# Performance work log

Hardware: AMD Instinct MI355X
Metric: run time of the kernel (lower is better)

The kernel has to match this reference:

```python
import jax, jax.numpy as jnp
import numpy as np

K_MAX, K_MIN = 12.0, 1.0
TEMP = 1.0
STE_ALPHA = 12.0
EPS = 1e-8

DIM, HID, KHID, WHID = 512, 2048, 128, 128
B, N = 8, 1024


def setup_inputs() -> dict:
    key = jax.random.key(0)
    ks = jax.random.split(key, 13)
    def lin(k, fan_in, shape):
        bound = 1.0 / np.sqrt(fan_in)
        return jax.random.uniform(k, shape, jnp.float32, -bound, bound)
    return {
        "x": jax.random.normal(ks[0], (B, N, DIM), jnp.float32),
        "fc1_w": lin(ks[1], DIM, (HID, DIM)),
        "fc1_b": lin(ks[2], DIM, (HID,)),
        "fc2_w": lin(ks[3], HID, (DIM, HID)),
        "fc2_b": lin(ks[4], HID, (DIM,)),
        "k1_w": lin(ks[5], DIM, (KHID, DIM)),
        "k1_b": lin(ks[6], DIM, (KHID,)),
        "k2_w": lin(ks[7], KHID, (3, KHID)),
        "k2_b": lin(ks[8], KHID, (3,)),
        "w1_w": lin(ks[9], DIM, (WHID, DIM)),
        "w1_b": lin(ks[10], DIM, (WHID,)),
        "w2_w": lin(ks[11], WHID, (3, WHID)),
        "w2_b": lin(ks[12], WHID, (3,)),
    }


def adaptive_knn_aggregate(h, k_cont):
    # h: (B,N,C), k_cont: (B,) continuous k in [k_min, k_max]
    sim = jnp.einsum("bnc,bmc->bnm", h, h) / TEMP          # (B,N,N)
    order = jnp.argsort(-sim, axis=-1)                      # descending
    rank = jnp.argsort(order, axis=-1).astype(h.dtype)      # rank 0 = most similar
    # soft top-k gate (STE-style sigmoid around k_cont)
    gate = jax.nn.sigmoid(STE_ALPHA * (k_cont[:, None, None] - (rank + 0.5)))
    attn = jax.nn.softmax(sim, axis=-1) * gate
    attn = attn / (attn.sum(axis=-1, keepdims=True) + EPS)
    return jnp.einsum("bnm,bmc->bnc", attn, h)


def reference(x, fc1_w, fc1_b, fc2_w, fc2_b, k1_w, k1_b, k2_w, k2_b,
              w1_w, w1_b, w2_w, w2_b):
    pooled = x.mean(axis=1)                                 # (B,C)
    # adaptive k values net
    kh = jax.nn.relu(pooled @ k1_w.T + k1_b)
    ratio = jax.nn.sigmoid(kh @ k2_w.T + k2_b)              # (B,3)
    k_cont = K_MIN + ratio * (K_MAX - K_MIN)
    # adaptive branch weights net
    wh = jax.nn.relu(pooled @ w1_w.T + w1_b)
    w = jax.nn.softmax(wh @ w2_w.T + w2_b, axis=-1)         # (B,3)
    # MLP (dropout p=0 -> identity)
    h = jax.nn.relu(x @ fc1_w.T + fc1_b)
    h = h @ fc2_w.T + fc2_b                                 # (B,N,C)
    # three KNN aggregation branches blended by w
    y = sum(adaptive_knn_aggregate(h, k_cont[:, i]) * w[:, i, None, None]
            for i in range(3))
    return y
```

## Files before the change

kernel.cpp:

```cpp
#include <hip/hip_runtime.h>
#include <math.h>

#define DIM_ 512
#define HID_ 2048
#define B_ 8
#define N_ 1024
#define ROWS_ 8192
#define TOPK 16

typedef __attribute__((ext_vector_type(8))) short short8;
typedef __attribute__((ext_vector_type(16))) float float16v;
typedef __attribute__((ext_vector_type(4))) float float4v;

__device__ __forceinline__ float sigm(float x) { return 1.f / (1.f + __expf(-x)); }

__device__ __forceinline__ short f2bf(float f) {
    unsigned u = __float_as_uint(f);
    u += 0x7FFF + ((u >> 16) & 1);
    return (short)(u >> 16);
}

__device__ __forceinline__ float bf2f(unsigned short s) {
    return __uint_as_float((unsigned)s << 16);
}

__device__ __forceinline__ unsigned f2ord(float f) {
    unsigned u = __float_as_uint(f);
    return (u & 0x80000000u) ? ~u : (u | 0x80000000u);
}

__device__ __forceinline__ unsigned dpp_xor1(unsigned v) {
    return (unsigned)__builtin_amdgcn_update_dpp(0, (int)v, 0xB1, 0xF, 0xF, true);
}
__device__ __forceinline__ unsigned dpp_xor2(unsigned v) {
    return (unsigned)__builtin_amdgcn_update_dpp(0, (int)v, 0x4E, 0xF, 0xF, true);
}
__device__ __forceinline__ unsigned sxr(unsigned v, int d) {
    if (d == 1) return dpp_xor1(v);
    if (d == 2) return dpp_xor2(v);
    return (unsigned)__shfl_xor((int)v, d);
}
__device__ __forceinline__ float sxrf(float v, int d) {
    return __uint_as_float(sxr(__float_as_uint(v), d));
}

__device__ __forceinline__ void gload16(const short* g, short* l) {
    __builtin_amdgcn_global_load_lds(
        (const __attribute__((address_space(1))) void*)g,
        (__attribute__((address_space(3))) void*)l, 16, 0, 0);
}

__global__ __launch_bounds__(512)
void prep_kernel(const float* __restrict__ x, float* __restrict__ part, short* __restrict__ xb,
                 const float* __restrict__ w1, const float* __restrict__ w2,
                 short* __restrict__ o1, short* __restrict__ o2) {
    const int bx = blockIdx.x;
    if (bx < 256) {
        const int b = bx >> 5, chunk = bx & 31;
        const int cg = (threadIdx.x & 127) * 4;
        const int rg = threadIdx.x >> 7;
        const long long rbase = (long long)b * N_ + chunk * 32 + rg * 8;
        const float* xp = x + rbase * DIM_ + cg;
        short* xo = xb + rbase * DIM_ + cg;
        float4 s = make_float4(0.f, 0.f, 0.f, 0.f);
#pragma unroll
        for (int n = 0; n < 8; ++n) {
            const float4 v = *(const float4*)(xp + (long long)n * DIM_);
            s.x += v.x; s.y += v.y; s.z += v.z; s.w += v.w;
            short4 o;
            o.x = f2bf(v.x); o.y = f2bf(v.y); o.z = f2bf(v.z); o.w = f2bf(v.w);
            *(short4*)(xo + (long long)n * DIM_) = o;
        }
        *(float4*)(part + ((long long)bx * 4 + rg) * DIM_ + cg) = s;
    } else {
        const int n4 = HID_ * DIM_ / 4;
        int i = (bx - 256) * 2048 + threadIdx.x;
#pragma unroll
        for (int t = 0; t < 4; ++t, i += 512) {
            const float* in = (i < n4) ? w1 : w2;
            short* out = (i < n4) ? o1 : o2;
            const int j = (i < n4) ? i : (i - n4);
            const float4 v = *(const float4*)(in + (long long)j * 4);
            short4 o;
            o.x = f2bf(v.x); o.y = f2bf(v.y); o.z = f2bf(v.z); o.w = f2bf(v.w);
            *(short4*)(out + (long long)j * 4) = o;
        }
    }
}

__global__ __launch_bounds__(512)
void pool_heads_kernel(const float* __restrict__ part,
                       const float* __restrict__ k1w, const float* __restrict__ k1b,
                       const float* __restrict__ k2w, const float* __restrict__ k2b,
                       const float* __restrict__ w1w, const float* __restrict__ w1b,
                       const float* __restrict__ w2w, const float* __restrict__ w2b,
                       float* __restrict__ kcont, float* __restrict__ wbr) {
    const int b = blockIdx.x;
    const int t = threadIdx.x;
    __shared__ float sp[DIM_];
    __shared__ float kh[128], wh[128];
    __shared__ float wraw[4];
    float s = 0.f;
    for (int g = 0; g < 128; ++g) s += part[((long long)b * 128 + g) * DIM_ + t];
    sp[t] = s * (1.f / 1024.f);
    __syncthreads();

    const int wv = t >> 6, l = t & 63;
    float sv[8];
    {
        const float4 a = *(const float4*)&sp[l * 8];
        const float4 c = *(const float4*)&sp[l * 8 + 4];
        sv[0] = a.x; sv[1] = a.y; sv[2] = a.z; sv[3] = a.w;
        sv[4] = c.x; sv[5] = c.y; sv[6] = c.z; sv[7] = c.w;
    }
#pragma unroll 4
    for (int i = 0; i < 16; ++i) {
        const int r = wv * 16 + i;
        const float4 k0 = *(const float4*)(k1w + (long long)r * DIM_ + l * 8);
        const float4 k1 = *(const float4*)(k1w + (long long)r * DIM_ + l * 8 + 4);
        const float4 q0 = *(const float4*)(w1w + (long long)r * DIM_ + l * 8);
        const float4 q1 = *(const float4*)(w1w + (long long)r * DIM_ + l * 8 + 4);
        float ak = sv[0] * k0.x;
        ak = fmaf(sv[1], k0.y, ak); ak = fmaf(sv[2], k0.z, ak); ak = fmaf(sv[3], k0.w, ak);
        ak = fmaf(sv[4], k1.x, ak); ak = fmaf(sv[5], k1.y, ak);
        ak = fmaf(sv[6], k1.z, ak); ak = fmaf(sv[7], k1.w, ak);
        float aw = sv[0] * q0.x;
        aw = fmaf(sv[1], q0.y, aw); aw = fmaf(sv[2], q0.z, aw); aw = fmaf(sv[3], q0.w, aw);
        aw = fmaf(sv[4], q1.x, aw); aw = fmaf(sv[5], q1.y, aw);
        aw = fmaf(sv[6], q1.z, aw); aw = fmaf(sv[7], q1.w, aw);
#pragma unroll
        for (int d = 32; d > 0; d >>= 1) {
            ak += __shfl_xor(ak, d);
            aw += __shfl_xor(aw, d);
        }
        if (l == 0) {
            kh[r] = fmaxf(ak + k1b[r], 0.f);
            wh[r] = fmaxf(aw + w1b[r], 0.f);
        }
    }
    __syncthreads();
    if (t < 3) {
        float rk = k2b[t], rw = w2b[t];
        for (int k = 0; k < 128; ++k) {
            rk = fmaf(kh[k], k2w[t * 128 + k], rk);
            rw = fmaf(wh[k], w2w[t * 128 + k], rw);
        }
        kcont[b * 3 + t] = 1.f + 11.f * sigm(rk);
        wraw[t] = rw;
    }
    __syncthreads();
    if (t == 0) {
        const float m = fmaxf(wraw[0], fmaxf(wraw[1], wraw[2]));
        const float e0 = __expf(wraw[0] - m), e1 = __expf(wraw[1] - m), e2 = __expf(wraw[2] - m);
        const float inv = 1.f / (e0 + e1 + e2);
        wbr[b * 3 + 0] = e0 * inv;
        wbr[b * 3 + 1] = e1 * inv;
        wbr[b * 3 + 2] = e2 * inv;
    }
}

template<int OUTMODE, int BN, int SWZ>
__global__ __launch_bounds__(256)
void gemm_mfma(const short* __restrict__ A, const short* __restrict__ Bm,
               const float* __restrict__ bias,
               float* __restrict__ outF, short* __restrict__ outB,
               int M, int N, int K, int lda, int ldb,
               long long sA, long long sB, long long sC) {
    constexpr int NJ = BN / 64;
    int bz, mi, ni;
    if (SWZ == 1) {
        const int id = blockIdx.x + gridDim.x * (blockIdx.y + gridDim.y * blockIdx.z);
        bz = id % gridDim.z;
        const int r = id / gridDim.z;
        ni = r % gridDim.x;
        mi = r / gridDim.x;
    } else {
        const int id = blockIdx.x + gridDim.x * blockIdx.y;
        const int numM = gridDim.y;
        const int mg = numM >> 3;
        bz = blockIdx.z;
        mi = (id & 7) * mg + (id >> 3) % mg;
        ni = id / numM;
    }
    A  += (long long)bz * sA;
    Bm += (long long)bz * sB;

    __shared__ short As[128 * 64];
    __shared__ short Bs[BN * 64];

    const int tid = threadIdx.x;
    const int lane = tid & 63;
    const int wv = tid >> 6;
    const int m0 = mi * 128;
    const int n0 = ni * BN;

    const int lrow = lane >> 3;
    const int cg = (lane & 7) ^ lrow;

    const int ml = (wv & 1) * 64;
    const int nl = (wv >> 1) * (BN / 2);
    const int fr = lane & 31;
    const int khh = lane >> 5;

    float16v acc[2][NJ];
#pragma unroll
    for (int i = 0; i < 2; ++i)
#pragma unroll
        for (int j = 0; j < NJ; ++j)
#pragma unroll
            for (int r = 0; r < 16; ++r) acc[i][j][r] = 0.f;

    for (int k0 = 0; k0 < K; k0 += 64) {
        __syncthreads();
#pragma unroll
        for (int i = 0; i < 4; ++i) {
            const int rloc = wv * 32 + i * 8 + lrow;
            gload16(A + (long long)(m0 + rloc) * lda + (k0 + cg * 8),
                    &As[(wv * 32 + i * 8) * 64]);
        }
#pragma unroll
        for (int i = 0; i < BN / 32; ++i) {
            const int rloc = wv * (BN / 4) + i * 8 + lrow;
            gload16(Bm + (long long)(n0 + rloc) * ldb + (k0 + cg * 8),
                    &Bs[(wv * (BN / 4) + i * 8) * 64]);
        }
        __syncthreads();
#pragma unroll
        for (int c = 0; c < 4; ++c) {
            const int ch = c * 2 + khh;
            short8 af[2], bfr[NJ];
#pragma unroll
            for (int i = 0; i < 2; ++i) {
                const int m = ml + i * 32 + fr;
                af[i] = *(const short8*)&As[m * 64 + ((ch ^ (m & 7)) * 8)];
            }
#pragma unroll
            for (int j = 0; j < NJ; ++j) {
                const int n = nl + j * 32 + fr;
                bfr[j] = *(const short8*)&Bs[n * 64 + ((ch ^ (n & 7)) * 8)];
            }
#pragma unroll
            for (int i = 0; i < 2; ++i)
#pragma unroll
                for (int j = 0; j < NJ; ++j)
                    acc[i][j] = __builtin_amdgcn_mfma_f32_32x32x16_bf16(
                        af[i], bfr[j], acc[i][j], 0, 0, 0);
        }
    }

    const long long outOfs = (long long)bz * sC;
#pragma unroll
    for (int i = 0; i < 2; ++i) {
#pragma unroll
        for (int j = 0; j < NJ; ++j) {
            const int ng = n0 + nl + j * 32 + fr;
            float bv = 0.f;
            if (OUTMODE != 2) bv = bias[ng];
#pragma unroll
            for (int r = 0; r < 16; ++r) {
                const int mg2 = m0 + ml + i * 32 + (r & 3) + 8 * (r >> 2) + 4 * khh;
                float v = acc[i][j][r] + bv;
                if (OUTMODE == 0) v = fmaxf(v, 0.f);
                const long long idx = outOfs + (long long)mg2 * N + ng;
                if (OUTMODE == 2) outF[idx] = v;
                else              outB[idx] = f2bf(v);
            }
        }
    }
}

template<int OUTMODE, bool BATCH>
__global__ __launch_bounds__(512, 2)
void gemm256(const short* __restrict__ A, const short* __restrict__ Bm,
             const float* __restrict__ bias, float* __restrict__ outF,
             short* __restrict__ outB, int M, int N, int K, int lda, int ldb,
             int mTiles, long long sA, long long sB, long long sC) {
    __shared__ short As[2][256 * 64];
    __shared__ short Bs[2][256 * 64];

    const int tid = threadIdx.x;
    const int lane = tid & 63;
    const int wv = tid >> 6;
    const int l15 = lane & 15;
    const int kq = lane >> 4;
    const int lr = lane >> 3;
    const int cg = (lane & 7) ^ lr;

    const int id = blockIdx.x;
    const int xcd = id & 7;
    const int r = id >> 3;
    int mi, ni;
    const short* Ag = A;
    const short* Bg = Bm;
    long long cOfs = 0;
    if (BATCH) {
        mi = r % mTiles; ni = r / mTiles;
        Ag += (long long)xcd * sA; Bg += (long long)xcd * sB; cOfs = (long long)xcd * sC;
    } else {
        const int mg = mTiles >> 3;
        mi = xcd * mg + r % mg; ni = r / mg;
    }
    const int m0 = mi * 256, n0 = ni * 256;
    const int wm = wv >> 2, wn = wv & 3;

    float4v acc[8][4];
#pragma unroll
    for (int i = 0; i < 8; ++i)
#pragma unroll
        for (int j = 0; j < 4; ++j)
#pragma unroll
            for (int q = 0; q < 4; ++q) acc[i][j][q] = 0.f;

    const int sB1 = (wv & 3) + (wv >> 2) * 8;

    auto stA = [&](int bf, int s, int k0) {
        gload16(Ag + (long long)(m0 + s * 8 + lr) * lda + (k0 + cg * 8), &As[bf][s * 8 * 64]);
    };
    auto stB = [&](int bf, int s, int k0) {
        gload16(Bg + (long long)(n0 + s * 8 + lr) * ldb + (k0 + cg * 8), &Bs[bf][s * 8 * 64]);
    };
    auto unit0 = [&](int bf, int k0) {
        stA(bf, wv, k0); stA(bf, 16 + wv, k0);
        stB(bf, sB1, k0); stB(bf, 16 + sB1, k0);
    };
    auto unit1 = [&](int bf, int k0) { stA(bf, 8 + wv, k0); stA(bf, 24 + wv, k0); };
    auto unit2 = [&](int bf, int k0) { stB(bf, 4 + sB1, k0); stB(bf, 20 + sB1, k0); };

    auto tile_body = [&](int bf, int k1, bool stage) {
#pragma unroll
        for (int p = 0; p < 4; ++p) {
            const int mq = p & 1, nq = p >> 1;
            short8 af[4][2], bfr[2][2];
#pragma unroll
            for (int f = 0; f < 4; ++f) {
                const int rA = wm * 128 + mq * 64 + f * 16 + l15;
                const int ro = rA * 64, sw = rA & 7;
#pragma unroll
                for (int ks = 0; ks < 2; ++ks)
                    af[f][ks] = *(const short8*)&As[bf][ro + (((ks * 4 + kq) ^ sw) * 8)];
            }
#pragma unroll
            for (int g = 0; g < 2; ++g) {
                const int rB = wn * 64 + nq * 32 + g * 16 + l15;
                const int ro = rB * 64, sw = rB & 7;
#pragma unroll
                for (int ks = 0; ks < 2; ++ks)
                    bfr[g][ks] = *(const short8*)&Bs[bf][ro + (((ks * 4 + kq) ^ sw) * 8)];
            }
            if (stage) {
                if (p == 0) unit0(bf ^ 1, k1);
                else if (p == 1) unit1(bf ^ 1, k1);
                else if (p == 2) unit2(bf ^ 1, k1);
                if (p == 0 || p == 1) asm volatile("s_waitcnt vmcnt(6)" ::: "memory");
                else if (p == 3)      asm volatile("s_waitcnt vmcnt(4)" ::: "memory");
            } else {
                if (p == 0)      asm volatile("s_waitcnt vmcnt(2)" ::: "memory");
                else if (p == 1) asm volatile("s_waitcnt vmcnt(0)" ::: "memory");
            }
            __builtin_amdgcn_s_barrier();
            asm volatile("s_waitcnt lgkmcnt(0)" ::: "memory");
            __builtin_amdgcn_sched_barrier(0);
            __builtin_amdgcn_s_setprio(1);
#pragma unroll
            for (int f = 0; f < 4; ++f)
#pragma unroll
                for (int g = 0; g < 2; ++g)
#pragma unroll
                    for (int ks = 0; ks < 2; ++ks)
                        acc[mq * 4 + f][nq * 2 + g] = __builtin_amdgcn_mfma_f32_16x16x32_bf16(
                            af[f][ks], bfr[g][ks], acc[mq * 4 + f][nq * 2 + g], 0, 0, 0);
            __builtin_amdgcn_s_setprio(0);
            if (stage || p < 3) __builtin_amdgcn_s_barrier();
        }
    };

    const int NT = K >> 6;
    unit0(0, 0);
    __builtin_amdgcn_sched_barrier(0);
    unit1(0, 0);
    __builtin_amdgcn_sched_barrier(0);
    unit2(0, 0);
    asm volatile("s_waitcnt vmcnt(4)" ::: "memory");
    __builtin_amdgcn_s_barrier();

    for (int t = 0; t < NT - 1; ++t)
        tile_body(t & 1, (t + 1) << 6, true);
    tile_body((NT - 1) & 1, 0, false);

#pragma unroll
    for (int mf = 0; mf < 8; ++mf) {
#pragma unroll
        for (int nf = 0; nf < 4; ++nf) {
            const int ng = n0 + wn * 64 + nf * 16 + l15;
            float bv = 0.f;
            if (OUTMODE != 2) bv = bias[ng];
            const int mb = m0 + wm * 128 + mf * 16 + kq * 4;
#pragma unroll
            for (int q = 0; q < 4; ++q) {
                float v = acc[mf][nf][q] + bv;
                if (OUTMODE == 0) v = fmaxf(v, 0.f);
                const long long idx = cOfs + (long long)(mb + q) * N + ng;
                if (OUTMODE == 2) outF[idx] = v;
                else              outB[idx] = f2bf(v);
            }
        }
    }
}

__global__ __launch_bounds__(256)
void topk_agg_kernel(const float* __restrict__ sim,
                     const float* __restrict__ kcont, const float* __restrict__ wbr,
                     const unsigned short* __restrict__ h, float* __restrict__ y) {
    const int wv = threadIdx.x >> 6;
    const int lane = threadIdx.x & 63;
    const int ll = lane & 15;
    const int id = blockIdx.x;
    const int b = id & 7;
    const int row = b * N_ + (id >> 3) * 4 + wv;
    const float* srow = sim + (long long)row * N_;

    const int base = lane * 16;
    float f[16];
#pragma unroll
    for (int q = 0; q < 4; ++q) {
        const float4 v = *(const float4*)(srow + base + q * 4);
        f[q * 4 + 0] = v.x; f[q * 4 + 1] = v.y; f[q * 4 + 2] = v.z; f[q * 4 + 3] = v.w;
    }

    float m = f[0];
#pragma unroll
    for (int j = 1; j < 16; ++j) m = fmaxf(m, f[j]);
#pragma unroll
    for (int d = 32; d > 0; d >>= 1) m = fmaxf(m, sxrf(m, d));
    const float maxv = m;

    float so = 0.f;
#pragma unroll
    for (int j = 0; j < 16; ++j) so += __expf(f[j] - maxv);
#pragma unroll
    for (int d = 32; d > 0; d >>= 1) so += sxrf(so, d);
    const float invden = 1.f / so;

    unsigned key[16];
#pragma unroll
    for (int j = 0; j < 16; ++j)
        key[j] = (f2ord(f[j]) & 0xFFFFFC00u) | (unsigned)(1023 - (base + j));

#pragma unroll
    for (int k = 2; k <= 16; k <<= 1) {
#pragma unroll
        for (int j = k >> 1; j > 0; j >>= 1) {
#pragma unroll
            for (int i = 0; i < 16; ++i) {
                const int l = i ^ j;
                if (l > i) {
                    const bool desc = ((i & k) == 0);
                    const unsigned a = key[i], bk = key[l];
                    const unsigned hi = (a > bk) ? a : bk;
                    const unsigned lo = (a > bk) ? bk : a;
                    key[i] = desc ? hi : lo;
                    key[l] = desc ? lo : hi;
                }
            }
        }
    }

#pragma unroll
    for (int d = 1; d < 64; d <<= 1) {
        unsigned o[16];
#pragma unroll
        for (int i = 0; i < 16; ++i) o[i] = sxr(key[15 - i], d);
#pragma unroll
        for (int i = 0; i < 16; ++i) key[i] = (key[i] > o[i]) ? key[i] : o[i];
#pragma unroll
        for (int j = 8; j > 0; j >>= 1) {
#pragma unroll
            for (int i = 0; i < 16; ++i) {
                if ((i & j) == 0) {
                    const unsigned a = key[i], bk = key[i | j];
                    key[i]     = (a > bk) ? a : bk;
                    key[i | j] = (a > bk) ? bk : a;
                }
            }
        }
    }

    unsigned k32 = 0;
#pragma unroll
    for (int j = 0; j < 16; ++j) k32 = (ll == j) ? key[j] : k32;
    const int myidx = 1023 - (int)(k32 & 1023u);
    const float myval = srow[myidx];

    unsigned long long kx = ((unsigned long long)f2ord(myval) << 32)
                          | (unsigned)(1023 - myidx);
#pragma unroll
    for (int k = 2; k <= 16; k <<= 1) {
#pragma unroll
        for (int d = k >> 1; d > 0; d >>= 1) {
            const unsigned olo = sxr((unsigned)kx, d);
            const unsigned ohi = sxr((unsigned)(kx >> 32), d);
            const unsigned long long other = ((unsigned long long)ohi << 32) | olo;
            const bool keepMax = (((ll & k) != 0) == ((ll & d) != 0));
            const bool mineBig = (kx > other);
            kx = (keepMax == mineBig) ? kx : other;
        }
    }
    const unsigned sord = (unsigned)(kx >> 32);
    const unsigned su = (sord & 0x80000000u) ? (sord & 0x7FFFFFFFu) : ~sord;
    const float sval = __uint_as_float(su);
    const int sidx = 1023 - (int)(kx & 1023u);

    const float kc0 = kcont[b * 3 + 0], kc1 = kcont[b * 3 + 1], kc2 = kcont[b * 3 + 2];
    const float w0 = wbr[b * 3 + 0], w1 = wbr[b * 3 + 1], w2 = wbr[b * 3 + 2];

    const float p = __expf(sval - maxv) * invden;
    const float rr = (float)ll + 0.5f;
    const float g0 = sigm(12.f * (kc0 - rr));
    const float g1 = sigm(12.f * (kc1 - rr));
    const float g2 = sigm(12.f * (kc2 - rr));
    float s0 = p * g0, s1 = p * g1, s2 = p * g2;
#pragma unroll
    for (int d = 1; d < 16; d <<= 1) {
        s0 += sxrf(s0, d);
        s1 += sxrf(s1, d);
        s2 += sxrf(s2, d);
    }
    const float f0 = w0 / (s0 + 1e-8f);
    const float f1 = w1 / (s1 + 1e-8f);
    const float f2 = w2 / (s2 + 1e-8f);
    const float mycoef = p * (f0 * g0 + f1 * g1 + f2 * g2);

    const unsigned short* hbase = h + (long long)b * (N_ * DIM_) + lane * 8;
    float acc[8] = {0.f, 0.f, 0.f, 0.f, 0.f, 0.f, 0.f, 0.f};
#pragma unroll
    for (int r = 0; r < TOPK; ++r) {
        const float c = __uint_as_float(
            (unsigned)__builtin_amdgcn_readlane((int)__float_as_uint(mycoef), r));
        const int   i = __builtin_amdgcn_readlane(sidx, r);
        const ushort4 a0 = *(const ushort4*)(hbase + (long long)i * DIM_);
        const ushort4 a1 = *(const ushort4*)(hbase + (long long)i * DIM_ + 4);
        acc[0] = fmaf(c, bf2f(a0.x), acc[0]);
        acc[1] = fmaf(c, bf2f(a0.y), acc[1]);
        acc[2] = fmaf(c, bf2f(a0.z), acc[2]);
        acc[3] = fmaf(c, bf2f(a0.w), acc[3]);
        acc[4] = fmaf(c, bf2f(a1.x), acc[4]);
        acc[5] = fmaf(c, bf2f(a1.y), acc[5]);
        acc[6] = fmaf(c, bf2f(a1.z), acc[6]);
        acc[7] = fmaf(c, bf2f(a1.w), acc[7]);
    }
    float* yp = y + (long long)row * DIM_ + lane * 8;
    *(float4*)(yp + 0) = make_float4(acc[0], acc[1], acc[2], acc[3]);
    *(float4*)(yp + 4) = make_float4(acc[4], acc[5], acc[6], acc[7]);
}

extern "C" void kernel_launch(void* const* d_in, const int* in_sizes, int n_in,
                              void* d_out, int out_size, void* d_ws, size_t ws_size,
                              hipStream_t stream) {
    const float* x     = (const float*)d_in[0];
    const float* fc1_w = (const float*)d_in[1];
    const float* fc1_b = (const float*)d_in[2];
    const float* fc2_w = (const float*)d_in[3];
    const float* fc2_b = (const float*)d_in[4];
    const float* k1_w  = (const float*)d_in[5];
    const float* k1_b  = (const float*)d_in[6];
    const float* k2_w  = (const float*)d_in[7];
    const float* k2_b  = (const float*)d_in[8];
    const float* w1_w  = (const float*)d_in[9];
    const float* w1_b  = (const float*)d_in[10];
    const float* w2_w  = (const float*)d_in[11];
    const float* w2_b  = (const float*)d_in[12];

    char* ws = (char*)d_ws;
    short* h1b    = (short*)(ws + 0);
    float* simbuf = (float*)(ws + 0);
    short* xb     = (short*)(ws + 33554432);
    short* hb     = (short*)(ws + 67108864);
    short* w1b    = (short*)(ws + 75497472);
    short* w2b    = (short*)(ws + 77594624);
    float* ppart  = (float*)(ws + 79691776);
    float* kcont  = (float*)(ws + 81788928);
    float* wbr    = (float*)(ws + 81789056);

    float* y = (float*)d_out;

    prep_kernel<<<dim3(512), dim3(512), 0, stream>>>(x, ppart, xb, fc1_w, fc2_w, w1b, w2b);
    pool_heads_kernel<<<dim3(B_), dim3(512), 0, stream>>>(ppart, k1_w, k1_b, k2_w, k2_b,
                                                          w1_w, w1_b, w2_w, w2_b, kcont, wbr);
    gemm256<0, false><<<dim3(256), dim3(512), 0, stream>>>(
        xb, w1b, fc1_b, nullptr, h1b, ROWS_, HID_, DIM_, DIM_, DIM_, 32, 0, 0, 0);
    gemm_mfma<1, 128, 2><<<dim3(DIM_ / 128, ROWS_ / 128, 1), dim3(256), 0, stream>>>(
        h1b, w2b, fc2_b, nullptr, hb, ROWS_, DIM_, HID_, HID_, HID_, 0, 0, 0);
    gemm_mfma<2, 128, 1><<<dim3(N_ / 128, N_ / 128, B_), dim3(256), 0, stream>>>(
        hb, hb, nullptr, simbuf, nullptr, N_, N_, DIM_, DIM_, DIM_,
        (long long)N_ * DIM_, (long long)N_ * DIM_, (long long)N_ * N_);
    topk_agg_kernel<<<dim3(ROWS_ / 4), dim3(256), 0, stream>>>(
        simbuf, kcont, wbr, (const unsigned short*)hb, y);
}
```

Measured before the change: 214.9 us.

## Replace 256-tile fc1 GEMM with generic MFMA kernel and shrink fc2 N-tile

Removes the hand-scheduled 256x256 double-buffered gemm256 kernel and runs fc1 with the generic gemm_mfma template using 128-wide tiles instead. fc2 now uses a 64-wide N tile, which doubles its grid from 256 to 512 blocks to fill more compute units. This trades fc1's larger-tile data reuse and explicit load/compute overlap for simpler code, and gives fc2 more parallelism at the cost of less reuse per block.

```diff
diff --git a/kernel.cpp b/kernel.cpp
--- a/kernel.cpp
+++ b/kernel.cpp
@@ -10,7 +10,6 @@
 
 typedef __attribute__((ext_vector_type(8))) short short8;
 typedef __attribute__((ext_vector_type(16))) float float16v;
-typedef __attribute__((ext_vector_type(4))) float float4v;
 
 __device__ __forceinline__ float sigm(float x) { return 1.f / (1.f + __expf(-x)); }
 
@@ -269,144 +268,6 @@
     }
 }
 
-template<int OUTMODE, bool BATCH>
-__global__ __launch_bounds__(512, 2)
-void gemm256(const short* __restrict__ A, const short* __restrict__ Bm,
-             const float* __restrict__ bias, float* __restrict__ outF,
-             short* __restrict__ outB, int M, int N, int K, int lda, int ldb,
-             int mTiles, long long sA, long long sB, long long sC) {
-    __shared__ short As[2][256 * 64];
-    __shared__ short Bs[2][256 * 64];
-
-    const int tid = threadIdx.x;
-    const int lane = tid & 63;
-    const int wv = tid >> 6;
-    const int l15 = lane & 15;
-    const int kq = lane >> 4;
-    const int lr = lane >> 3;
-    const int cg = (lane & 7) ^ lr;
-
-    const int id = blockIdx.x;
-    const int xcd = id & 7;
-    const int r = id >> 3;
-    int mi, ni;
-    const short* Ag = A;
-    const short* Bg = Bm;
-    long long cOfs = 0;
-    if (BATCH) {
-        mi = r % mTiles; ni = r / mTiles;
-        Ag += (long long)xcd * sA; Bg += (long long)xcd * sB; cOfs = (long long)xcd * sC;
-    } else {
-        const int mg = mTiles >> 3;
-        mi = xcd * mg + r % mg; ni = r / mg;
-    }
-    const int m0 = mi * 256, n0 = ni * 256;
-    const int wm = wv >> 2, wn = wv & 3;
-
-    float4v acc[8][4];
-#pragma unroll
-    for (int i = 0; i < 8; ++i)
-#pragma unroll
-        for (int j = 0; j < 4; ++j)
-#pragma unroll
-            for (int q = 0; q < 4; ++q) acc[i][j][q] = 0.f;
-
-    const int sB1 = (wv & 3) + (wv >> 2) * 8;
-
-    auto stA = [&](int bf, int s, int k0) {
-        gload16(Ag + (long long)(m0 + s * 8 + lr) * lda + (k0 + cg * 8), &As[bf][s * 8 * 64]);
-    };
-    auto stB = [&](int bf, int s, int k0) {
-        gload16(Bg + (long long)(n0 + s * 8 + lr) * ldb + (k0 + cg * 8), &Bs[bf][s * 8 * 64]);
-    };
-    auto unit0 = [&](int bf, int k0) {
-        stA(bf, wv, k0); stA(bf, 16 + wv, k0);
-        stB(bf, sB1, k0); stB(bf, 16 + sB1, k0);
-    };
-    auto unit1 = [&](int bf, int k0) { stA(bf, 8 + wv, k0); stA(bf, 24 + wv, k0); };
-    auto unit2 = [&](int bf, int k0) { stB(bf, 4 + sB1, k0); stB(bf, 20 + sB1, k0); };
-
-    auto tile_body = [&](int bf, int k1, bool stage) {
-#pragma unroll
-        for (int p = 0; p < 4; ++p) {
-            const int mq = p & 1, nq = p >> 1;
-            short8 af[4][2], bfr[2][2];
-#pragma unroll
-            for (int f = 0; f < 4; ++f) {
-                const int rA = wm * 128 + mq * 64 + f * 16 + l15;
-                const int ro = rA * 64, sw = rA & 7;
-#pragma unroll
-                for (int ks = 0; ks < 2; ++ks)
-                    af[f][ks] = *(const short8*)&As[bf][ro + (((ks * 4 + kq) ^ sw) * 8)];
-            }
-#pragma unroll
-            for (int g = 0; g < 2; ++g) {
-                const int rB = wn * 64 + nq * 32 + g * 16 + l15;
-                const int ro = rB * 64, sw = rB & 7;
-#pragma unroll
-                for (int ks = 0; ks < 2; ++ks)
-                    bfr[g][ks] = *(const short8*)&Bs[bf][ro + (((ks * 4 + kq) ^ sw) * 8)];
-            }
-            if (stage) {
-                if (p == 0) unit0(bf ^ 1, k1);
-                else if (p == 1) unit1(bf ^ 1, k1);
-                else if (p == 2) unit2(bf ^ 1, k1);
-                if (p == 0 || p == 1) asm volatile("s_waitcnt vmcnt(6)" ::: "memory");
-                else if (p == 3)      asm volatile("s_waitcnt vmcnt(4)" ::: "memory");
-            } else {
-                if (p == 0)      asm volatile("s_waitcnt vmcnt(2)" ::: "memory");
-                else if (p == 1) asm volatile("s_waitcnt vmcnt(0)" ::: "memory");
-            }
-            __builtin_amdgcn_s_barrier();
-            asm volatile("s_waitcnt lgkmcnt(0)" ::: "memory");
-            __builtin_amdgcn_sched_barrier(0);
-            __builtin_amdgcn_s_setprio(1);
-#pragma unroll
-            for (int f = 0; f < 4; ++f)
-#pragma unroll
-                for (int g = 0; g < 2; ++g)
-#pragma unroll
-                    for (int ks = 0; ks < 2; ++ks)
-                        acc[mq * 4 + f][nq * 2 + g] = __builtin_amdgcn_mfma_f32_16x16x32_bf16(
-                            af[f][ks], bfr[g][ks], acc[mq * 4 + f][nq * 2 + g], 0, 0, 0);
-            __builtin_amdgcn_s_setprio(0);
-            if (stage || p < 3) __builtin_amdgcn_s_barrier();
-        }
-    };
-
-    const int NT = K >> 6;
-    unit0(0, 0);
-    __builtin_amdgcn_sched_barrier(0);
-    unit1(0, 0);
-    __builtin_amdgcn_sched_barrier(0);
-    unit2(0, 0);
-    asm volatile("s_waitcnt vmcnt(4)" ::: "memory");
-    __builtin_amdgcn_s_barrier();
-
-    for (int t = 0; t < NT - 1; ++t)
-        tile_body(t & 1, (t + 1) << 6, true);
-    tile_body((NT - 1) & 1, 0, false);
-
-#pragma unroll
-    for (int mf = 0; mf < 8; ++mf) {
-#pragma unroll
-        for (int nf = 0; nf < 4; ++nf) {
-            const int ng = n0 + wn * 64 + nf * 16 + l15;
-            float bv = 0.f;
-            if (OUTMODE != 2) bv = bias[ng];
-            const int mb = m0 + wm * 128 + mf * 16 + kq * 4;
-#pragma unroll
-            for (int q = 0; q < 4; ++q) {
-                float v = acc[mf][nf][q] + bv;
-                if (OUTMODE == 0) v = fmaxf(v, 0.f);
-                const long long idx = cOfs + (long long)(mb + q) * N + ng;
-                if (OUTMODE == 2) outF[idx] = v;
-                else              outB[idx] = f2bf(v);
-            }
-        }
-    }
-}
-
 __global__ __launch_bounds__(256)
 void topk_agg_kernel(const float* __restrict__ sim,
                      const float* __restrict__ kcont, const float* __restrict__ wbr,
@@ -586,9 +447,9 @@
     prep_kernel<<<dim3(512), dim3(512), 0, stream>>>(x, ppart, xb, fc1_w, fc2_w, w1b, w2b);
     pool_heads_kernel<<<dim3(B_), dim3(512), 0, stream>>>(ppart, k1_w, k1_b, k2_w, k2_b,
                                                           w1_w, w1_b, w2_w, w2_b, kcont, wbr);
-    gemm256<0, false><<<dim3(256), dim3(512), 0, stream>>>(
-        xb, w1b, fc1_b, nullptr, h1b, ROWS_, HID_, DIM_, DIM_, DIM_, 32, 0, 0, 0);
-    gemm_mfma<1, 128, 2><<<dim3(DIM_ / 128, ROWS_ / 128, 1), dim3(256), 0, stream>>>(
+    gemm_mfma<0, 128, 2><<<dim3(HID_ / 128, ROWS_ / 128, 1), dim3(256), 0, stream>>>(
+        xb, w1b, fc1_b, nullptr, h1b, ROWS_, HID_, DIM_, DIM_, DIM_, 0, 0, 0);
+    gemm_mfma<1, 64, 2><<<dim3(DIM_ / 64, ROWS_ / 128, 1), dim3(256), 0, stream>>>(
         h1b, w2b, fc2_b, nullptr, hb, ROWS_, DIM_, HID_, HID_, HID_, 0, 0, 0);
     gemm_mfma<2, 128, 1><<<dim3(N_ / 128, N_ / 128, B_), dim3(256), 0, stream>>>(
         hb, hb, nullptr, simbuf, nullptr, N_, N_, DIM_, DIM_, DIM_,
```

New measurement: 210.9 us. About the same (-1.9%).
